# Kernel tuning notes

Hardware: AMD Instinct MI355X
Metric: run time of the kernel (lower is better)

Reference implementation:

```python
import jax, jax.numpy as jnp
import numpy as np
import math

N, IN_DIM, Z, H, OUT, K = 16384, 64, 128, 1, 3, 16


def setup_inputs() -> dict:
    key = jax.random.key(0)
    ks = jax.random.split(key, 16)

    def lin(k, din, dout):
        kw, kb = jax.random.split(k)
        W = jax.random.normal(kw, (din, dout), jnp.float32) / math.sqrt(din)
        b = jax.random.normal(kb, (dout,), jnp.float32) * 0.01
        return W, b

    x = jax.random.normal(ks[0], (N, IN_DIM), jnp.float32)
    t = jnp.zeros((1,), jnp.float32)
    # layer dims: (in, heads*out) per TransformerConv
    dims = [(IN_DIM, Z * H), (Z * H, (Z // H) * H), (Z * H, (OUT // H) * H)]
    params = {}
    i = 1
    for li, (din, dout) in enumerate(dims, 1):
        for nm in ("q", "k", "v", "s"):
            W, b = lin(ks[i], din, dout)
            i += 1
            params[f"W{nm}{li}"] = W
            params[f"b{nm}{li}"] = b
    return {"t": t, "x": x, **params}


def knn_edge_index(coo, k):
    # kNN graph on 3-D coords (loop=False): edges neighbor(src) -> center(dst)
    n = coo.shape[0]
    sq = jnp.sum(coo * coo, axis=-1)
    d = sq[:, None] + sq[None, :] - 2.0 * (coo @ coo.T)  # [N, N] sq. distances
    d = d.at[jnp.arange(n), jnp.arange(n)].set(jnp.inf)  # exclude self-loops
    _, idx = jax.lax.top_k(-d, k)  # [N, K] nearest neighbor indices
    src = idx.reshape(-1)
    dst = jnp.repeat(jnp.arange(n), k)
    return src, dst


def tconv(x, src, dst, Wq, bq, Wk, bk, Wv, bv, Ws, bs, heads):
    # PyG TransformerConv (concat=True, root_weight=True, no edge_attr)
    n = x.shape[0]
    dout = Wq.shape[1]
    c = dout // heads
    q = (x @ Wq + bq).reshape(n, heads, c)
    kk = (x @ Wk + bk).reshape(n, heads, c)
    v = (x @ Wv + bv).reshape(n, heads, c)
    alpha = jnp.sum(q[dst] * kk[src], axis=-1) / math.sqrt(c)  # [E, H]
    amax = jax.ops.segment_max(alpha, dst, num_segments=n)
    ex = jnp.exp(alpha - amax[dst])
    denom = jax.ops.segment_sum(ex, dst, num_segments=n)
    w = ex / denom[dst]  # softmax over incoming edges per node
    msg = w[:, :, None] * v[src]  # [E, H, C]
    out = jax.ops.segment_sum(msg, dst, num_segments=n).reshape(n, dout)
    return out + x @ Ws + bs  # root/skip connection


def reference(t, x,
              Wq1, bq1, Wk1, bk1, Wv1, bv1, Ws1, bs1,
              Wq2, bq2, Wk2, bk2, Wv2, bv2, Ws2, bs2,
              Wq3, bq3, Wk3, bk3, Wv3, bv3, Ws3, bs3):
    src, dst = knn_edge_index(x[:, :3], K)  # built under no_grad in original
    h = jnp.tanh(tconv(x, src, dst, Wq1, bq1, Wk1, bk1, Wv1, bv1, Ws1, bs1, H))
    h = jnp.tanh(tconv(h, src, dst, Wq2, bq2, Wk2, bk2, Wv2, bv2, Ws2, bs2, H) + h)
    drift_coo = tconv(h, src, dst, Wq3, bq3, Wk3, bk3, Wv3, bv3, Ws3, bs3, H)
    return drift_coo
```

## Files before the change

kernel.cpp:

```cpp
#include <hip/hip_runtime.h>
#include <math.h>

#define NN 16384
#define QPW 2
#define CAP 128
#define WM 64
#define KTOP 17

typedef unsigned long long u64;

__global__ __launch_bounds__(256) void pack_coords(const float* __restrict__ x,
                                                   float4* __restrict__ coo) {
  int i = blockIdx.x * 256 + threadIdx.x;
  float a = x[i * 64 + 0];
  float b = x[i * 64 + 1];
  float c = x[i * 64 + 2];
  coo[i] = make_float4(a, b, c, -0.5f * (a * a + b * b + c * c));
}

__device__ __forceinline__ int mbcnt64(u64 mask) {
  return __builtin_amdgcn_mbcnt_hi(
      (unsigned)(mask >> 32),
      __builtin_amdgcn_mbcnt_lo((unsigned)mask, 0));
}

__device__ __forceinline__ unsigned fmap(float d) {
  unsigned ub = __float_as_uint(d);
  return ub ^ ((unsigned)((int)ub >> 31) | 0x80000000u);
}

__device__ __forceinline__ float unfmap(unsigned ub) {
  unsigned fb = (ub & 0x80000000u) ? (ub ^ 0x80000000u) : ~ub;
  return __uint_as_float(fb);
}

__device__ __forceinline__ unsigned short f2bf(float f) {
  unsigned u = __float_as_uint(f);
  return (unsigned short)((u + 0x7FFFu + ((u >> 16) & 1u)) >> 16);
}
__device__ __forceinline__ float bf2f(unsigned short h) {
  return __uint_as_float(((unsigned)h) << 16);
}

__device__ __forceinline__ u64 u64min(u64 a, u64 b) { return a < b ? a : b; }
__device__ __forceinline__ u64 u64max(u64 a, u64 b) { return a > b ? a : b; }

__device__ __forceinline__ void sort128(u64& r0, u64& r1, int lane) {
#pragma unroll
  for (int k = 2; k <= 128; k <<= 1) {
    if (k == 128) {
      u64 lo = u64min(r0, r1);
      r1 = u64max(r0, r1);
      r0 = lo;
    }
#pragma unroll
    for (int jj = (k == 128 ? 32 : (k >> 1)); jj >= 1; jj >>= 1) {
      const bool up = (lane & jj) == 0;
      const bool asc0 = (lane & k) == 0;
      const bool asc1 = ((lane | 64) & k) == 0;
      u64 o0 = __shfl_xor(r0, jj);
      u64 o1 = __shfl_xor(r1, jj);
      r0 = (up == asc0) ? u64min(r0, o0) : u64max(r0, o0);
      r1 = (up == asc1) ? u64min(r1, o1) : u64max(r1, o1);
    }
  }
}

__device__ __forceinline__ void radix_shrink(u64* buf, int& cnt, float& cq,
                                             int lane) {
  const u64 k0 = (lane < cnt) ? buf[lane] : ~0ull;
  const u64 k1 = (lane + 64 < cnt) ? buf[lane + 64] : ~0ull;
  const unsigned d0 = (unsigned)(k0 >> 32);
  const unsigned d1 = (unsigned)(k1 >> 32);
  unsigned p = 0u;
#pragma unroll
  for (int b = 31; b >= 0; --b) {
    const unsigned c = p | (1u << b);
    const u64 b0 = __ballot(d0 < c);
    const u64 b1 = __ballot(d1 < c);
    const int n = __popcll(b0) + __popcll(b1);
    if (n < KTOP) p = c;
  }
  const bool v0 = d0 <= p;
  const bool v1 = d1 <= p;
  const u64 m0 = __ballot(v0);
  const u64 m1 = __ballot(v1);
  const int base = __popcll(m0);
  if (v0) buf[mbcnt64(m0)] = k0;
  if (v1) buf[base + mbcnt64(m1)] = k1;
  cnt = base + __popcll(m1);
  cq = -unfmap(p);
}

__global__ __launch_bounds__(256) void knn_kernel(const float4* __restrict__ coo,
                                                  int* __restrict__ src) {
  __shared__ u64 bufs[4][QPW][CAP];
  const int lane = threadIdx.x & 63;
  const int wid = threadIdx.x >> 6;
  const int node0 = blockIdx.x * (4 * QPW) + wid * QPW;

  float qx[QPW], qy[QPW], qz[QPW], cq[QPW];
  int cnt[QPW];
#pragma unroll
  for (int q = 0; q < QPW; ++q) {
    const float4 me = coo[node0 + q];
    qx[q] = me.x;
    qy[q] = me.y;
    qz[q] = me.z;
    cnt[q] = 0;
  }

  {
    const float4 pa = coo[lane];
    const float4 pb = coo[64 + lane];
#pragma unroll
    for (int q = 0; q < QPW; ++q) {
      const float L0 = fmaf(qx[q], pa.x,
                        fmaf(qy[q], pa.y, fmaf(qz[q], pa.z, pa.w)));
      const float L1 = fmaf(qx[q], pb.x,
                        fmaf(qy[q], pb.y, fmaf(qz[q], pb.z, pb.w)));
      bufs[wid][q][lane] = ((u64)fmap(-L0) << 32) | (unsigned)lane;
      bufs[wid][q][64 + lane] = ((u64)fmap(-L1) << 32) | (unsigned)(64 + lane);
      cnt[q] = 128;
      radix_shrink(bufs[wid][q], cnt[q], cq[q], lane);
    }
  }

  float4 s0 = coo[2 * 64 + lane];
  float4 s1 = coo[3 * 64 + lane];
  float4 s2 = coo[4 * 64 + lane];
  float4 s3 = coo[5 * 64 + lane];

  auto body = [&](const float4 cur, const int step) {
    const int j = step * 64 + lane;
    float L[QPW];
#pragma unroll
    for (int q = 0; q < QPW; ++q)
      L[q] = fmaf(qx[q], cur.x,
                  fmaf(qy[q], cur.y, fmaf(qz[q], cur.z, cur.w)));
    u64 mk[QPW];
#pragma unroll
    for (int q = 0; q < QPW; ++q) mk[q] = __ballot(L[q] >= cq[q]);
    if (mk[0] | mk[1]) {
#pragma unroll
      for (int q = 0; q < QPW; ++q) {
        if (mk[q]) {
          if (L[q] >= cq[q])
            bufs[wid][q][cnt[q] + mbcnt64(mk[q])] =
                ((u64)fmap(-L[q]) << 32) | (unsigned)j;
          cnt[q] += __popcll(mk[q]);
          if (cnt[q] >= WM) radix_shrink(bufs[wid][q], cnt[q], cq[q], lane);
        }
      }
    }
  };

#pragma unroll 1
  for (int g = 0; g < 63; ++g) {
    const int base = 2 + g * 4;
    body(s0, base + 0);
    s0 = coo[(base + 4) * 64 + lane];
    body(s1, base + 1);
    s1 = coo[(base + 5) * 64 + lane];
    body(s2, base + 2);
    s2 = coo[(base + 6) * 64 + lane];
    body(s3, base + 3);
    s3 = coo[(base + 7) * 64 + lane];
  }
  body(s0, 254);
  body(s1, 255);

#pragma unroll 1
  for (int q = 0; q < QPW; ++q) {
    u64 r0 = (lane < cnt[q]) ? bufs[wid][q][lane] : ~0ull;
    u64 r1 = (lane + 64 < cnt[q]) ? bufs[wid][q][lane + 64] : ~0ull;
    sort128(r0, r1, lane);
    const int idx = (int)(r0 & 0xFFFFFFFFull);
    const u64 selfm = __ballot((lane < KTOP) && (idx == node0 + q));
    const int s = selfm ? (__ffsll((long long)selfm) - 1) : 99;
    const int outrank = lane - (lane > s ? 1 : 0);
    if (lane < KTOP && lane != s && outrank < 16)
      src[(node0 + q) * 16 + outrank] = idx;
  }
}

template <int KD>
__global__ __launch_bounds__(256) void gemm_qkvs(
    const float* __restrict__ X, const float* __restrict__ W0,
    const float* __restrict__ W1, const float* __restrict__ W2,
    const float* __restrict__ W3, const float* __restrict__ B0,
    const float* __restrict__ B1, const float* __restrict__ B2,
    const float* __restrict__ B3, float* __restrict__ qs,
    unsigned short* __restrict__ kvh) {
  __shared__ float As[64][68];
  __shared__ float Bs[64][64];
  const int brow = blockIdx.x * 64;
  const int by = blockIdx.y;
  const int wi = by >> 1;
  const float* W = wi == 0 ? W0 : wi == 1 ? W1 : wi == 2 ? W2 : W3;
  const float* bias = wi == 0 ? B0 : wi == 1 ? B1 : wi == 2 ? B2 : B3;
  const int cbase = (by & 1) * 64;
  const int tx = threadIdx.x & 15;
  const int ty = threadIdx.x >> 4;

  float acc[4][4] = {};
  for (int k0 = 0; k0 < KD; k0 += 64) {
    __syncthreads();
#pragma unroll
    for (int i = 0; i < 4; ++i) {
      const int flat = threadIdx.x * 4 + i * 1024;
      const int r = flat >> 6, kk = flat & 63;
      const float4 v = *(const float4*)&X[(brow + r) * KD + k0 + kk];
      As[kk + 0][r] = v.x;
      As[kk + 1][r] = v.y;
      As[kk + 2][r] = v.z;
      As[kk + 3][r] = v.w;
    }
#pragma unroll
    for (int i = 0; i < 4; ++i) {
      const int flat = threadIdx.x * 4 + i * 1024;
      const int kk = flat >> 6, c = flat & 63;
      *(float4*)&Bs[kk][c] = *(const float4*)&W[(k0 + kk) * 128 + cbase + c];
    }
    __syncthreads();
#pragma unroll 8
    for (int k = 0; k < 64; ++k) {
      const float4 a = *(const float4*)&As[k][ty * 4];
      const float4 b = *(const float4*)&Bs[k][tx * 4];
      const float av[4] = {a.x, a.y, a.z, a.w};
      const float bv[4] = {b.x, b.y, b.z, b.w};
#pragma unroll
      for (int i = 0; i < 4; ++i)
#pragma unroll
        for (int jj = 0; jj < 4; ++jj)
          acc[i][jj] = fmaf(av[i], bv[jj], acc[i][jj]);
    }
  }
  const float4 bi = *(const float4*)&bias[cbase + tx * 4];
  const int col = cbase + tx * 4;
#pragma unroll
  for (int i = 0; i < 4; ++i) {
    const int row = brow + ty * 4 + i;
    float4 o;
    o.x = acc[i][0] + bi.x;
    o.y = acc[i][1] + bi.y;
    o.z = acc[i][2] + bi.z;
    o.w = acc[i][3] + bi.w;
    if (wi == 0) {
      *(float4*)&qs[row * 256 + col] = o;
    } else if (wi == 3) {
      *(float4*)&qs[row * 256 + 128 + col] = o;
    } else {
      ushort4 h;
      h.x = f2bf(o.x);
      h.y = f2bf(o.y);
      h.z = f2bf(o.z);
      h.w = f2bf(o.w);
      *(ushort4*)&kvh[row * 256 + (wi == 1 ? col : 128 + col)] = h;
    }
  }
}

__global__ __launch_bounds__(256) void attn_c128(
    const float* __restrict__ qs, const unsigned short* __restrict__ kvh,
    const int* __restrict__ src, const float* __restrict__ res,
    float* __restrict__ hout, int do_res) {
  const int g = threadIdx.x >> 5;
  const int node = blockIdx.x * 8 + g;
  const int c = threadIdx.x & 31;
  const float4 q4 = ((const float4*)(qs + node * 256))[c];

  int nb[16];
#pragma unroll
  for (int r = 0; r < 16; ++r) nb[r] = src[node * 16 + r];

  float p[16];
#pragma unroll
  for (int r = 0; r < 16; ++r) {
    const ushort4 k4 = ((const ushort4*)(kvh + nb[r] * 256))[c];
    p[r] = q4.x * bf2f(k4.x) + q4.y * bf2f(k4.y) + q4.z * bf2f(k4.z) +
           q4.w * bf2f(k4.w);
  }
#pragma unroll
  for (int o = 16; o; o >>= 1) {
#pragma unroll
    for (int r = 0; r < 16; ++r) p[r] += __shfl_xor(p[r], o);
  }

  float m = p[0];
#pragma unroll
  for (int r = 1; r < 16; ++r) m = fmaxf(m, p[r]);
  float w[16];
  float den = 0.0f;
#pragma unroll
  for (int r = 0; r < 16; ++r) {
    w[r] = __expf((p[r] - m) * 0.088388347648318447f);
    den += w[r];
  }
  const float inv = 1.0f / den;
  float o0 = 0.0f, o1 = 0.0f, o2 = 0.0f, o3 = 0.0f;
#pragma unroll
  for (int r = 0; r < 16; ++r) {
    const ushort4 v4 = ((const ushort4*)(kvh + nb[r] * 256 + 128))[c];
    const float ww = w[r] * inv;
    o0 = fmaf(ww, bf2f(v4.x), o0);
    o1 = fmaf(ww, bf2f(v4.y), o1);
    o2 = fmaf(ww, bf2f(v4.z), o2);
    o3 = fmaf(ww, bf2f(v4.w), o3);
  }
  const float4 s4 = ((const float4*)(qs + node * 256 + 128))[c];
  float r0 = o0 + s4.x, r1 = o1 + s4.y, r2 = o2 + s4.z, r3 = o3 + s4.w;
  if (do_res) {
    const float4 h4 = ((const float4*)(res + node * 128))[c];
    r0 += h4.x;
    r1 += h4.y;
    r2 += h4.z;
    r3 += h4.w;
  }
  ((float4*)(hout + node * 128))[c] =
      make_float4(tanhf(r0), tanhf(r1), tanhf(r2), tanhf(r3));
}

__global__ __launch_bounds__(256) void gemm_qkvs3(
    const float* __restrict__ H, const float* __restrict__ W0,
    const float* __restrict__ W1, const float* __restrict__ W2,
    const float* __restrict__ W3, const float* __restrict__ B0,
    const float* __restrict__ B1, const float* __restrict__ B2,
    const float* __restrict__ B3, float* __restrict__ out) {
  __shared__ float hs[64][132];
  __shared__ float wsh[128 * 12];
  __shared__ float bsh[12];
  const int brow = blockIdx.x * 64;
  if (threadIdx.x < 12) {
    const int mi = threadIdx.x / 3, c = threadIdx.x % 3;
    const float* Bsel = mi == 0 ? B0 : mi == 1 ? B1 : mi == 2 ? B2 : B3;
    bsh[threadIdx.x] = Bsel[c];
  }
  for (int t = threadIdx.x; t < 1536; t += 256) {
    const int k = t / 12, cc = t % 12;
    const int mi = cc / 3, c = cc % 3;
    const float* Wsel = mi == 0 ? W0 : mi == 1 ? W1 : mi == 2 ? W2 : W3;
    wsh[t] = Wsel[k * 3 + c];
  }
#pragma unroll
  for (int i = 0; i < 8; ++i) {
    const int flat = threadIdx.x * 4 + i * 1024;
    const int r = flat >> 7, kk = flat & 127;
    *(float4*)&hs[r][kk] = *(const float4*)&H[(brow + r) * 128 + kk];
  }
  __syncthreads();
  const int r = threadIdx.x >> 2;
  const int part = threadIdx.x & 3;
  float a0 = 0.0f, a1 = 0.0f, a2 = 0.0f;
#pragma unroll 4
  for (int k = 0; k < 128; ++k) {
    const float h = hs[r][k];
    a0 = fmaf(h, wsh[k * 12 + part * 3 + 0], a0);
    a1 = fmaf(h, wsh[k * 12 + part * 3 + 1], a1);
    a2 = fmaf(h, wsh[k * 12 + part * 3 + 2], a2);
  }
  const int row = brow + r;
  out[row * 12 + part * 3 + 0] = a0 + bsh[part * 3 + 0];
  out[row * 12 + part * 3 + 1] = a1 + bsh[part * 3 + 1];
  out[row * 12 + part * 3 + 2] = a2 + bsh[part * 3 + 2];
}

__global__ __launch_bounds__(256) void attn_c3(const float* __restrict__ q3,
                                               const int* __restrict__ src,
                                               float* __restrict__ out) {
  const int gid = blockIdx.x * 256 + threadIdx.x;
  const int node = gid >> 4, r = gid & 15;
  const int j = src[node * 16 + r];
  const float* qn = q3 + node * 12;
  const float* kj = q3 + j * 12 + 3;
  float alpha = (qn[0] * kj[0] + qn[1] * kj[1] + qn[2] * kj[2]) *
                0.57735026918962576f;
  float m = alpha;
#pragma unroll
  for (int o = 8; o; o >>= 1) m = fmaxf(m, __shfl_xor(m, o, 16));
  const float e = __expf(alpha - m);
  float den = e;
#pragma unroll
  for (int o = 8; o; o >>= 1) den += __shfl_xor(den, o, 16);
  const float wgt = e / den;
  const float* vj = q3 + j * 12 + 6;
  float o0 = wgt * vj[0], o1 = wgt * vj[1], o2 = wgt * vj[2];
#pragma unroll
  for (int o = 8; o; o >>= 1) {
    o0 += __shfl_xor(o0, o, 16);
    o1 += __shfl_xor(o1, o, 16);
    o2 += __shfl_xor(o2, o, 16);
  }
  if (r == 0) {
    const float* sn = q3 + node * 12 + 9;
    out[node * 3 + 0] = o0 + sn[0];
    out[node * 3 + 1] = o1 + sn[1];
    out[node * 3 + 2] = o2 + sn[2];
  }
}

extern "C" void kernel_launch(void* const* d_in, const int* in_sizes, int n_in,
                              void* d_out, int out_size, void* d_ws,
                              size_t ws_size, hipStream_t stream) {
  const float* x = (const float*)d_in[1];
  const float* Wq1 = (const float*)d_in[2];
  const float* bq1 = (const float*)d_in[3];
  const float* Wk1 = (const float*)d_in[4];
  const float* bk1 = (const float*)d_in[5];
  const float* Wv1 = (const float*)d_in[6];
  const float* bv1 = (const float*)d_in[7];
  const float* Ws1 = (const float*)d_in[8];
  const float* bs1 = (const float*)d_in[9];
  const float* Wq2 = (const float*)d_in[10];
  const float* bq2 = (const float*)d_in[11];
  const float* Wk2 = (const float*)d_in[12];
  const float* bk2 = (const float*)d_in[13];
  const float* Wv2 = (const float*)d_in[14];
  const float* bv2 = (const float*)d_in[15];
  const float* Ws2 = (const float*)d_in[16];
  const float* bs2 = (const float*)d_in[17];
  const float* Wq3 = (const float*)d_in[18];
  const float* bq3 = (const float*)d_in[19];
  const float* Wk3 = (const float*)d_in[20];
  const float* bk3 = (const float*)d_in[21];
  const float* Wv3 = (const float*)d_in[22];
  const float* bv3 = (const float*)d_in[23];
  const float* Ws3 = (const float*)d_in[24];
  const float* bs3 = (const float*)d_in[25];

  const size_t MB = 1024 * 1024;
  char* ws = (char*)d_ws;
  float* qs = (float*)(ws);
  unsigned short* kvh = (unsigned short*)(ws + 16 * MB);
  float* h1 = (float*)(ws + 24 * MB);
  float* h2 = (float*)(ws + 32 * MB);
  int* src = (int*)(ws + 40 * MB);
  float4* coo = (float4*)(ws + 41 * MB);
  float* q3 = (float*)(ws + 42 * MB);
  float* out = (float*)d_out;

  pack_coords<<<NN / 256, 256, 0, stream>>>(x, coo);
  knn_kernel<<<NN / (4 * QPW), 256, 0, stream>>>(coo, src);
  gemm_qkvs<64><<<dim3(NN / 64, 8), 256, 0, stream>>>(
      x, Wq1, Wk1, Wv1, Ws1, bq1, bk1, bv1, bs1, qs, kvh);
  attn_c128<<<NN / 8, 256, 0, stream>>>(qs, kvh, src, nullptr, h1, 0);
  gemm_qkvs<128><<<dim3(NN / 64, 8), 256, 0, stream>>>(
      h1, Wq2, Wk2, Wv2, Ws2, bq2, bk2, bv2, bs2, qs, kvh);
  attn_c128<<<NN / 8, 256, 0, stream>>>(qs, kvh, src, h1, h2, 1);
  gemm_qkvs3<<<NN / 64, 256, 0, stream>>>(h2, Wq3, Wk3, Wv3, Ws3, bq3, bk3,
                                          bv3, bs3, q3);
  attn_c3<<<NN * 16 / 256, 256, 0, stream>>>(q3, src, out);
}
```

Baseline: 299.5 us.

## Replace brute-force kNN with uniform-grid spatial binning and expanding-shell search

Replaces the all-pairs kNN scan with a 32^3 uniform grid over the 3-D coordinates. Points are histogrammed, prefix-summed and scattered into cell order. Each wave then searches expanding shells of cells around its query until the 17th-nearest distance bound is covered. This is meant to remove the O(N^2) distance evaluation that dominated the graph build, at the cost of several extra small kernels, atomics and data-dependent loop divergence. Ties between equal distances may now be broken by visit order rather than by index, and the fixed grid extent of [-4,4) assumes a roughly normal coordinate distribution.

```diff
diff --git a/kernel.cpp b/kernel.cpp
--- a/kernel.cpp
+++ b/kernel.cpp
@@ -2,21 +2,13 @@
 #include <math.h>
 
 #define NN 16384
-#define QPW 2
 #define CAP 128
 #define WM 64
 #define KTOP 17
+#define GRD 32
+#define GH 0.25f
 
 typedef unsigned long long u64;
-
-__global__ __launch_bounds__(256) void pack_coords(const float* __restrict__ x,
-                                                   float4* __restrict__ coo) {
-  int i = blockIdx.x * 256 + threadIdx.x;
-  float a = x[i * 64 + 0];
-  float b = x[i * 64 + 1];
-  float c = x[i * 64 + 2];
-  coo[i] = make_float4(a, b, c, -0.5f * (a * a + b * b + c * c));
-}
 
 __device__ __forceinline__ int mbcnt64(u64 mask) {
   return __builtin_amdgcn_mbcnt_hi(
@@ -45,23 +37,20 @@
 __device__ __forceinline__ u64 u64min(u64 a, u64 b) { return a < b ? a : b; }
 __device__ __forceinline__ u64 u64max(u64 a, u64 b) { return a > b ? a : b; }
 
-__device__ __forceinline__ void sort128(u64& r0, u64& r1, int lane) {
-#pragma unroll
-  for (int k = 2; k <= 128; k <<= 1) {
-    if (k == 128) {
-      u64 lo = u64min(r0, r1);
-      r1 = u64max(r0, r1);
-      r0 = lo;
-    }
-#pragma unroll
-    for (int jj = (k == 128 ? 32 : (k >> 1)); jj >= 1; jj >>= 1) {
+__device__ __forceinline__ int cellc(float v) {
+  int c = (int)floorf((v + 4.0f) * 4.0f);
+  return c < 0 ? 0 : (c > GRD - 1 ? GRD - 1 : c);
+}
+
+__device__ __forceinline__ void sort64(u64& r0, int lane) {
+#pragma unroll
+  for (int k = 2; k <= 64; k <<= 1) {
+#pragma unroll
+    for (int jj = k >> 1; jj >= 1; jj >>= 1) {
       const bool up = (lane & jj) == 0;
-      const bool asc0 = (lane & k) == 0;
-      const bool asc1 = ((lane | 64) & k) == 0;
-      u64 o0 = __shfl_xor(r0, jj);
-      u64 o1 = __shfl_xor(r1, jj);
-      r0 = (up == asc0) ? u64min(r0, o0) : u64max(r0, o0);
-      r1 = (up == asc1) ? u64min(r1, o1) : u64max(r1, o1);
+      const bool asc = (lane & k) == 0;
+      u64 o = __shfl_xor(r0, jj);
+      r0 = (up == asc) ? u64min(r0, o) : u64max(r0, o);
     }
   }
 }
@@ -92,96 +81,136 @@
   cq = -unfmap(p);
 }
 
-__global__ __launch_bounds__(256) void knn_kernel(const float4* __restrict__ coo,
-                                                  int* __restrict__ src) {
-  __shared__ u64 bufs[4][QPW][CAP];
+__global__ __launch_bounds__(256) void pack_cells(const float* __restrict__ x,
+                                                  float4* __restrict__ tmp4,
+                                                  int* __restrict__ cid,
+                                                  unsigned* __restrict__ hist) {
+  const int i = blockIdx.x * 256 + threadIdx.x;
+  const float a = x[i * 64 + 0];
+  const float b = x[i * 64 + 1];
+  const float c = x[i * 64 + 2];
+  tmp4[i] = make_float4(a, b, c, -0.5f * (a * a + b * b + c * c));
+  const int cell = (cellc(c) * GRD + cellc(b)) * GRD + cellc(a);
+  cid[i] = cell;
+  atomicAdd(&hist[cell], 1u);
+}
+
+__global__ __launch_bounds__(1024) void prefix_cells(
+    const unsigned* __restrict__ hist, unsigned* __restrict__ cellstart,
+    unsigned* __restrict__ cellfill) {
+  __shared__ unsigned ls[1024];
+  const int t = threadIdx.x;
+  unsigned s = 0;
+  for (int k = 0; k < 32; ++k) s += hist[t * 32 + k];
+  ls[t] = s;
+  __syncthreads();
+  for (int off = 1; off < 1024; off <<= 1) {
+    const unsigned v = (t >= off) ? ls[t - off] : 0u;
+    __syncthreads();
+    ls[t] += v;
+    __syncthreads();
+  }
+  unsigned run = ls[t] - s;
+  for (int k = 0; k < 32; ++k) {
+    cellstart[t * 32 + k] = run;
+    cellfill[t * 32 + k] = run;
+    run += hist[t * 32 + k];
+  }
+  if (t == 1023) cellstart[GRD * GRD * GRD] = run;
+}
+
+__global__ __launch_bounds__(256) void scatter_cells(
+    const float4* __restrict__ tmp4, const int* __restrict__ cid,
+    unsigned* __restrict__ cellfill, float4* __restrict__ sorted4,
+    int* __restrict__ sidx) {
+  const int i = blockIdx.x * 256 + threadIdx.x;
+  const unsigned pos = atomicAdd(&cellfill[cid[i]], 1u);
+  sorted4[pos] = tmp4[i];
+  sidx[pos] = i;
+}
+
+__global__ __launch_bounds__(256) void knn_grid(
+    const float4* __restrict__ sorted4, const int* __restrict__ sidx,
+    const unsigned* __restrict__ cellstart, int* __restrict__ src) {
+  __shared__ u64 bufs_[4][CAP];
   const int lane = threadIdx.x & 63;
   const int wid = threadIdx.x >> 6;
-  const int node0 = blockIdx.x * (4 * QPW) + wid * QPW;
-
-  float qx[QPW], qy[QPW], qz[QPW], cq[QPW];
-  int cnt[QPW];
-#pragma unroll
-  for (int q = 0; q < QPW; ++q) {
-    const float4 me = coo[node0 + q];
-    qx[q] = me.x;
-    qy[q] = me.y;
-    qz[q] = me.z;
-    cnt[q] = 0;
-  }
-
-  {
-    const float4 pa = coo[lane];
-    const float4 pb = coo[64 + lane];
-#pragma unroll
-    for (int q = 0; q < QPW; ++q) {
-      const float L0 = fmaf(qx[q], pa.x,
-                        fmaf(qy[q], pa.y, fmaf(qz[q], pa.z, pa.w)));
-      const float L1 = fmaf(qx[q], pb.x,
-                        fmaf(qy[q], pb.y, fmaf(qz[q], pb.z, pb.w)));
-      bufs[wid][q][lane] = ((u64)fmap(-L0) << 32) | (unsigned)lane;
-      bufs[wid][q][64 + lane] = ((u64)fmap(-L1) << 32) | (unsigned)(64 + lane);
-      cnt[q] = 128;
-      radix_shrink(bufs[wid][q], cnt[q], cq[q], lane);
-    }
-  }
-
-  float4 s0 = coo[2 * 64 + lane];
-  float4 s1 = coo[3 * 64 + lane];
-  float4 s2 = coo[4 * 64 + lane];
-  float4 s3 = coo[5 * 64 + lane];
-
-  auto body = [&](const float4 cur, const int step) {
-    const int j = step * 64 + lane;
-    float L[QPW];
-#pragma unroll
-    for (int q = 0; q < QPW; ++q)
-      L[q] = fmaf(qx[q], cur.x,
-                  fmaf(qy[q], cur.y, fmaf(qz[q], cur.z, cur.w)));
-    u64 mk[QPW];
-#pragma unroll
-    for (int q = 0; q < QPW; ++q) mk[q] = __ballot(L[q] >= cq[q]);
-    if (mk[0] | mk[1]) {
-#pragma unroll
-      for (int q = 0; q < QPW; ++q) {
-        if (mk[q]) {
-          if (L[q] >= cq[q])
-            bufs[wid][q][cnt[q] + mbcnt64(mk[q])] =
-                ((u64)fmap(-L[q]) << 32) | (unsigned)j;
-          cnt[q] += __popcll(mk[q]);
-          if (cnt[q] >= WM) radix_shrink(bufs[wid][q], cnt[q], cq[q], lane);
+  u64* buf = bufs_[wid];
+  const int qpos = blockIdx.x * 4 + wid;
+  const float4 me = sorted4[qpos];
+  const int qorig = sidx[qpos];
+  const float qx = me.x, qy = me.y, qz = me.z;
+  const float myq2 = -2.0f * me.w;
+  const int cx = cellc(qx), cy = cellc(qy), cz = cellc(qz);
+  float cq = -INFINITY;
+  int cnt = 0;
+
+  auto scan_run = [&](int xa, int xb, int y, int z) {
+    const int x0 = xa < 0 ? 0 : xa;
+    const int x1 = xb > GRD - 1 ? GRD - 1 : xb;
+    if (x0 > x1) return;
+    const int c0 = (z * GRD + y) * GRD + x0;
+    const int s = (int)cellstart[c0];
+    const int e = (int)cellstart[c0 + (x1 - x0) + 1];
+    for (int o = s; o < e; o += 64) {
+      const int j = o + lane;
+      const bool in = j < e;
+      const float4 p = sorted4[in ? j : s];
+      const float L = fmaf(qx, p.x, fmaf(qy, p.y, fmaf(qz, p.z, p.w)));
+      const bool pass = in && (L >= cq);
+      const u64 mk = __ballot(pass);
+      if (mk) {
+        if (pass)
+          buf[cnt + mbcnt64(mk)] =
+              ((u64)fmap(-L) << 32) | (unsigned)sidx[j];
+        cnt += __popcll(mk);
+        if (cnt >= WM) radix_shrink(buf, cnt, cq, lane);
+      }
+    }
+  };
+
+  int rho_done = -1;
+  int rho_t = 1;
+  while (true) {
+    for (int dz = -rho_t; dz <= rho_t; ++dz) {
+      const int z = cz + dz;
+      if ((unsigned)z > (unsigned)(GRD - 1)) continue;
+      const int adz = dz < 0 ? -dz : dz;
+      for (int dy = -rho_t; dy <= rho_t; ++dy) {
+        const int y = cy + dy;
+        if ((unsigned)y > (unsigned)(GRD - 1)) continue;
+        const int ady = dy < 0 ? -dy : dy;
+        const int m = adz > ady ? adz : ady;
+        if (m > rho_done) {
+          scan_run(cx - rho_t, cx + rho_t, y, z);
+        } else {
+          scan_run(cx - rho_t, cx - rho_done - 1, y, z);
+          scan_run(cx + rho_done + 1, cx + rho_t, y, z);
         }
       }
     }
-  };
-
-#pragma unroll 1
-  for (int g = 0; g < 63; ++g) {
-    const int base = 2 + g * 4;
-    body(s0, base + 0);
-    s0 = coo[(base + 4) * 64 + lane];
-    body(s1, base + 1);
-    s1 = coo[(base + 5) * 64 + lane];
-    body(s2, base + 2);
-    s2 = coo[(base + 6) * 64 + lane];
-    body(s3, base + 3);
-    s3 = coo[(base + 7) * 64 + lane];
-  }
-  body(s0, 254);
-  body(s1, 255);
-
-#pragma unroll 1
-  for (int q = 0; q < QPW; ++q) {
-    u64 r0 = (lane < cnt[q]) ? bufs[wid][q][lane] : ~0ull;
-    u64 r1 = (lane + 64 < cnt[q]) ? bufs[wid][q][lane + 64] : ~0ull;
-    sort128(r0, r1, lane);
-    const int idx = (int)(r0 & 0xFFFFFFFFull);
-    const u64 selfm = __ballot((lane < KTOP) && (idx == node0 + q));
-    const int s = selfm ? (__ffsll((long long)selfm) - 1) : 99;
-    const int outrank = lane - (lane > s ? 1 : 0);
-    if (lane < KTOP && lane != s && outrank < 16)
-      src[(node0 + q) * 16 + outrank] = idx;
-  }
+    rho_done = rho_t;
+    if (cnt >= KTOP) {
+      radix_shrink(buf, cnt, cq, lane);
+      const float d17 = fmaxf(myq2 - 2.0f * cq, 0.0f);
+      const float need = sqrtf(d17 * 1.000002f + 1e-12f) * (1.0f / GH);
+      if ((float)rho_done >= need || rho_done >= GRD) break;
+      int rn = (int)need + 1;
+      rho_t = rn > rho_done + 1 ? rn : rho_done + 1;
+      if (rho_t > GRD) rho_t = GRD;
+    } else {
+      rho_t = rho_done + 1;
+    }
+  }
+
+  u64 r0 = (lane < cnt) ? buf[lane] : ~0ull;
+  sort64(r0, lane);
+  const int idx = (int)(r0 & 0xFFFFFFFFull);
+  const u64 selfm = __ballot((lane < KTOP) && (idx == qorig));
+  const int sp = selfm ? (__ffsll((long long)selfm) - 1) : 99;
+  const int outrank = lane - (lane > sp ? 1 : 0);
+  if (lane < KTOP && lane != sp && outrank < 16)
+    src[qorig * 16 + outrank] = idx;
 }
 
 template <int KD>
@@ -429,18 +458,30 @@
   const float* bs3 = (const float*)d_in[25];
 
   const size_t MB = 1024 * 1024;
+  const size_t KB = 1024;
   char* ws = (char*)d_ws;
+  float4* tmp4 = (float4*)(ws);
+  float4* sorted4 = (float4*)(ws + 256 * KB);
+  int* cid = (int*)(ws + 512 * KB);
+  int* sidx = (int*)(ws + 576 * KB);
+  unsigned* hist = (unsigned*)(ws + 640 * KB);
+  unsigned* cellstart = (unsigned*)(ws + 768 * KB);
+  unsigned* cellfill = (unsigned*)(ws + 904 * KB);
+
   float* qs = (float*)(ws);
   unsigned short* kvh = (unsigned short*)(ws + 16 * MB);
   float* h1 = (float*)(ws + 24 * MB);
   float* h2 = (float*)(ws + 32 * MB);
   int* src = (int*)(ws + 40 * MB);
-  float4* coo = (float4*)(ws + 41 * MB);
   float* q3 = (float*)(ws + 42 * MB);
   float* out = (float*)d_out;
 
-  pack_coords<<<NN / 256, 256, 0, stream>>>(x, coo);
-  knn_kernel<<<NN / (4 * QPW), 256, 0, stream>>>(coo, src);
+  hipMemsetAsync(hist, 0, GRD * GRD * GRD * sizeof(unsigned), stream);
+  pack_cells<<<NN / 256, 256, 0, stream>>>(x, tmp4, cid, hist);
+  prefix_cells<<<1, 1024, 0, stream>>>(hist, cellstart, cellfill);
+  scatter_cells<<<NN / 256, 256, 0, stream>>>(tmp4, cid, cellfill, sorted4,
+                                              sidx);
+  knn_grid<<<NN / 4, 256, 0, stream>>>(sorted4, sidx, cellstart, src);
   gemm_qkvs<64><<<dim3(NN / 64, 8), 256, 0, stream>>>(
       x, Wq1, Wk1, Wv1, Ws1, bq1, bk1, bv1, bs1, qs, kvh);
   attn_c128<<<NN / 8, 256, 0, stream>>>(qs, kvh, src, nullptr, h1, 0);
```

New measurement: 427.2 us. 42.6% more time.

## Reorder nodes by z-slab so attention gathers hit neighboring rows

Applied to the files above, without the earlier changes.

Buckets nodes by their z coordinate into 128 slabs using a histogram, a prefix scan and an atomic scatter, then renumbers nodes by slab rank. The kNN output, the layer-1 GEMM outputs and all later layers use the permuted order, and the final output is scattered back to original indices. This is meant to improve cache locality of the neighbor gathers in the attention kernels. It adds three small kernels and a memset, and the atomic scatter makes the ordering nondeterministic within a slab.

```diff
diff --git a/kernel.cpp b/kernel.cpp
--- a/kernel.cpp
+++ b/kernel.cpp
@@ -6,17 +6,10 @@
 #define CAP 128
 #define WM 64
 #define KTOP 17
+#define NSLAB 128
+#define SHI 16.0f
 
 typedef unsigned long long u64;
-
-__global__ __launch_bounds__(256) void pack_coords(const float* __restrict__ x,
-                                                   float4* __restrict__ coo) {
-  int i = blockIdx.x * 256 + threadIdx.x;
-  float a = x[i * 64 + 0];
-  float b = x[i * 64 + 1];
-  float c = x[i * 64 + 2];
-  coo[i] = make_float4(a, b, c, -0.5f * (a * a + b * b + c * c));
-}
 
 __device__ __forceinline__ int mbcnt64(u64 mask) {
   return __builtin_amdgcn_mbcnt_hi(
@@ -44,6 +37,11 @@
 
 __device__ __forceinline__ u64 u64min(u64 a, u64 b) { return a < b ? a : b; }
 __device__ __forceinline__ u64 u64max(u64 a, u64 b) { return a > b ? a : b; }
+
+__device__ __forceinline__ int slabof(float v) {
+  int c = (int)floorf((v + 4.0f) * SHI);
+  return c < 0 ? 0 : (c > NSLAB - 1 ? NSLAB - 1 : c);
+}
 
 __device__ __forceinline__ void sort128(u64& r0, u64& r1, int lane) {
 #pragma unroll
@@ -92,8 +90,48 @@
   cq = -unfmap(p);
 }
 
+__global__ __launch_bounds__(256) void pack_all(const float* __restrict__ x,
+                                                float4* __restrict__ coo,
+                                                int* __restrict__ sid,
+                                                unsigned* __restrict__ hist) {
+  const int i = blockIdx.x * 256 + threadIdx.x;
+  const float a = x[i * 64 + 0];
+  const float b = x[i * 64 + 1];
+  const float c = x[i * 64 + 2];
+  coo[i] = make_float4(a, b, c, -0.5f * (a * a + b * b + c * c));
+  const int s = slabof(c);
+  sid[i] = s;
+  atomicAdd(&hist[s], 1u);
+}
+
+__global__ __launch_bounds__(128) void prefix_slabs(
+    const unsigned* __restrict__ hist, unsigned* __restrict__ slabfill) {
+  __shared__ unsigned ls[NSLAB];
+  const int t = threadIdx.x;
+  const unsigned h = hist[t];
+  ls[t] = h;
+  __syncthreads();
+  for (int off = 1; off < NSLAB; off <<= 1) {
+    const unsigned v = (t >= off) ? ls[t - off] : 0u;
+    __syncthreads();
+    ls[t] += v;
+    __syncthreads();
+  }
+  slabfill[t] = ls[t] - h;
+}
+
+__global__ __launch_bounds__(256) void rank_scatter(
+    const int* __restrict__ sid, unsigned* __restrict__ slabfill,
+    int* __restrict__ sidx, int* __restrict__ rank) {
+  const int i = blockIdx.x * 256 + threadIdx.x;
+  const int pos = (int)atomicAdd(&slabfill[sid[i]], 1u);
+  sidx[pos] = i;
+  rank[i] = pos;
+}
+
 __global__ __launch_bounds__(256) void knn_kernel(const float4* __restrict__ coo,
-                                                  int* __restrict__ src) {
+                                                  const int* __restrict__ rank,
+                                                  int* __restrict__ srcs) {
   __shared__ u64 bufs[4][QPW][CAP];
   const int lane = threadIdx.x & 63;
   const int wid = threadIdx.x >> 6;
@@ -179,8 +217,9 @@
     const u64 selfm = __ballot((lane < KTOP) && (idx == node0 + q));
     const int s = selfm ? (__ffsll((long long)selfm) - 1) : 99;
     const int outrank = lane - (lane > s ? 1 : 0);
+    const int qsp = rank[node0 + q];
     if (lane < KTOP && lane != s && outrank < 16)
-      src[(node0 + q) * 16 + outrank] = idx;
+      srcs[qsp * 16 + outrank] = rank[idx];
   }
 }
 
@@ -190,8 +229,8 @@
     const float* __restrict__ W1, const float* __restrict__ W2,
     const float* __restrict__ W3, const float* __restrict__ B0,
     const float* __restrict__ B1, const float* __restrict__ B2,
-    const float* __restrict__ B3, float* __restrict__ qs,
-    unsigned short* __restrict__ kvh) {
+    const float* __restrict__ B3, const int* __restrict__ rmap,
+    float* __restrict__ qs, unsigned short* __restrict__ kvh) {
   __shared__ float As[64][68];
   __shared__ float Bs[64][64];
   const int brow = blockIdx.x * 64;
@@ -241,29 +280,30 @@
 #pragma unroll
   for (int i = 0; i < 4; ++i) {
     const int row = brow + ty * 4 + i;
+    const int orow = rmap ? rmap[row] : row;
     float4 o;
     o.x = acc[i][0] + bi.x;
     o.y = acc[i][1] + bi.y;
     o.z = acc[i][2] + bi.z;
     o.w = acc[i][3] + bi.w;
     if (wi == 0) {
-      *(float4*)&qs[row * 256 + col] = o;
+      *(float4*)&qs[orow * 256 + col] = o;
     } else if (wi == 3) {
-      *(float4*)&qs[row * 256 + 128 + col] = o;
+      *(float4*)&qs[orow * 256 + 128 + col] = o;
     } else {
       ushort4 h;
       h.x = f2bf(o.x);
       h.y = f2bf(o.y);
       h.z = f2bf(o.z);
       h.w = f2bf(o.w);
-      *(ushort4*)&kvh[row * 256 + (wi == 1 ? col : 128 + col)] = h;
+      *(ushort4*)&kvh[orow * 256 + (wi == 1 ? col : 128 + col)] = h;
     }
   }
 }
 
 __global__ __launch_bounds__(256) void attn_c128(
     const float* __restrict__ qs, const unsigned short* __restrict__ kvh,
-    const int* __restrict__ src, const float* __restrict__ res,
+    const int* __restrict__ srcs, const float* __restrict__ res,
     float* __restrict__ hout, int do_res) {
   const int g = threadIdx.x >> 5;
   const int node = blockIdx.x * 8 + g;
@@ -272,7 +312,7 @@
 
   int nb[16];
 #pragma unroll
-  for (int r = 0; r < 16; ++r) nb[r] = src[node * 16 + r];
+  for (int r = 0; r < 16; ++r) nb[r] = srcs[node * 16 + r];
 
   float p[16];
 #pragma unroll
@@ -366,11 +406,12 @@
 }
 
 __global__ __launch_bounds__(256) void attn_c3(const float* __restrict__ q3,
-                                               const int* __restrict__ src,
+                                               const int* __restrict__ srcs,
+                                               const int* __restrict__ sidx,
                                                float* __restrict__ out) {
   const int gid = blockIdx.x * 256 + threadIdx.x;
   const int node = gid >> 4, r = gid & 15;
-  const int j = src[node * 16 + r];
+  const int j = srcs[node * 16 + r];
   const float* qn = q3 + node * 12;
   const float* kj = q3 + j * 12 + 3;
   float alpha = (qn[0] * kj[0] + qn[1] * kj[1] + qn[2] * kj[2]) *
@@ -393,9 +434,10 @@
   }
   if (r == 0) {
     const float* sn = q3 + node * 12 + 9;
-    out[node * 3 + 0] = o0 + sn[0];
-    out[node * 3 + 1] = o1 + sn[1];
-    out[node * 3 + 2] = o2 + sn[2];
+    const int onode = sidx[node];
+    out[onode * 3 + 0] = o0 + sn[0];
+    out[onode * 3 + 1] = o1 + sn[1];
+    out[onode * 3 + 2] = o2 + sn[2];
   }
 }
 
@@ -429,25 +471,34 @@
   const float* bs3 = (const float*)d_in[25];
 
   const size_t MB = 1024 * 1024;
+  const size_t KB = 1024;
   char* ws = (char*)d_ws;
   float* qs = (float*)(ws);
   unsigned short* kvh = (unsigned short*)(ws + 16 * MB);
   float* h1 = (float*)(ws + 24 * MB);
   float* h2 = (float*)(ws + 32 * MB);
-  int* src = (int*)(ws + 40 * MB);
+  int* srcs = (int*)(ws + 40 * MB);
   float4* coo = (float4*)(ws + 41 * MB);
+  int* sid = (int*)(ws + 41 * MB + 320 * KB);
+  int* sidx = (int*)(ws + 41 * MB + 384 * KB);
+  int* rank = (int*)(ws + 41 * MB + 448 * KB);
+  unsigned* hist = (unsigned*)(ws + 41 * MB + 512 * KB);
+  unsigned* slabfill = (unsigned*)(ws + 41 * MB + 514 * KB);
   float* q3 = (float*)(ws + 42 * MB);
   float* out = (float*)d_out;
 
-  pack_coords<<<NN / 256, 256, 0, stream>>>(x, coo);
-  knn_kernel<<<NN / (4 * QPW), 256, 0, stream>>>(coo, src);
+  hipMemsetAsync(hist, 0, NSLAB * sizeof(unsigned), stream);
+  pack_all<<<NN / 256, 256, 0, stream>>>(x, coo, sid, hist);
+  prefix_slabs<<<1, NSLAB, 0, stream>>>(hist, slabfill);
+  rank_scatter<<<NN / 256, 256, 0, stream>>>(sid, slabfill, sidx, rank);
+  knn_kernel<<<NN / (4 * QPW), 256, 0, stream>>>(coo, rank, srcs);
   gemm_qkvs<64><<<dim3(NN / 64, 8), 256, 0, stream>>>(
-      x, Wq1, Wk1, Wv1, Ws1, bq1, bk1, bv1, bs1, qs, kvh);
-  attn_c128<<<NN / 8, 256, 0, stream>>>(qs, kvh, src, nullptr, h1, 0);
+      x, Wq1, Wk1, Wv1, Ws1, bq1, bk1, bv1, bs1, rank, qs, kvh);
+  attn_c128<<<NN / 8, 256, 0, stream>>>(qs, kvh, srcs, nullptr, h1, 0);
   gemm_qkvs<128><<<dim3(NN / 64, 8), 256, 0, stream>>>(
-      h1, Wq2, Wk2, Wv2, Ws2, bq2, bk2, bv2, bs2, qs, kvh);
-  attn_c128<<<NN / 8, 256, 0, stream>>>(qs, kvh, src, h1, h2, 1);
+      h1, Wq2, Wk2, Wv2, Ws2, bq2, bk2, bv2, bs2, nullptr, qs, kvh);
+  attn_c128<<<NN / 8, 256, 0, stream>>>(qs, kvh, srcs, h1, h2, 1);
   gemm_qkvs3<<<NN / 64, 256, 0, stream>>>(h2, Wq3, Wk3, Wv3, Ws3, bq3, bk3,
                                           bv3, bs3, q3);
-  attn_c3<<<NN * 16 / 256, 256, 0, stream>>>(q3, src, out);
-}
+  attn_c3<<<NN * 16 / 256, 256, 0, stream>>>(q3, srcs, sidx, out);
+}
```

Result: slower. 342.2 us (+14.2%).
